# Optimization experiments

Hardware: AMD Instinct MI355X
Metric: run time of the kernel (lower is better)

Reference implementation:

```python
import jax, jax.numpy as jnp
import numpy as np

K = 10            # top-k patches
NUM_SAMPLES = 500 # perturbation samples
SIGMA = 0.05
PATCH = 128       # patch_size


def _perturbed_topk_core(x, noise):
    d = x.shape[-1]
    perturbed = x[:, None, :] + noise * SIGMA          # (b, n, d)
    _, idx = jax.lax.top_k(perturbed, K)               # (b, n, k)
    idx = jnp.sort(idx, axis=-1)
    onehot = jax.nn.one_hot(idx, d, dtype=x.dtype)     # (b, n, k, d)
    return onehot.mean(axis=1), onehot


@jax.custom_vjp
def perturbed_topk(x):
    noise = jax.random.normal(jax.random.key(1), (x.shape[0], NUM_SAMPLES, x.shape[1]), x.dtype)
    ind, _ = _perturbed_topk_core(x, noise)
    return ind


def _ptopk_fwd(x):
    noise = jax.random.normal(jax.random.key(1), (x.shape[0], NUM_SAMPLES, x.shape[1]), x.dtype)
    ind, onehot = _perturbed_topk_core(x, noise)
    return ind, (onehot, noise)


def _ptopk_bwd(res, g):
    onehot, noise = res
    # faithful to PerturbedTopKFunction.backward, fused to avoid the (b,k,d,e) tensor
    gx = jnp.einsum('bkd,bnkd,bne->be', g, onehot, noise) * (K / (NUM_SAMPLES * SIGMA))
    return (gx,)


perturbed_topk.defvjp(_ptopk_fwd, _ptopk_bwd)


def _forward(x_high, scores_2d):
    b, c, H, W = x_high.shape
    hs, ws = scores_2d.shape[1], scores_2d.shape[2]
    scores_1d = scores_2d.reshape(b, hs * ws)
    # entropy of softmax scores (torch.special.entr(p).sum(-1).mean(0))
    logp = jax.nn.log_softmax(scores_1d, axis=-1)
    p = jnp.exp(logp)
    entr = (-(p * logp).sum(-1)).mean()
    # min-max normalize
    smin = scores_1d.min(axis=-1, keepdims=True)
    smax = scores_1d.max(axis=-1, keepdims=True)
    norm = (scores_1d - smin) / (smax - smin + 1e-5)
    ind = perturbed_topk(norm).reshape(b, K, hs, ws)
    # padding identical to the torch code
    scale_h, scale_w = H // hs, W // ws
    padded_h = scale_h * hs + PATCH - 1
    padded_w = scale_w * ws + PATCH - 1
    top = (PATCH - scale_h) // 2
    left = (PATCH - scale_w) // 2
    bottom = padded_h - top - H
    right = padded_w - left - W
    x_pad = jnp.pad(x_high, ((0, 0), (0, 0), (top, bottom), (left, right)))
    # vectorized replacement of the nested i/j patch-accumulation loop
    row_idx = jnp.arange(hs)[:, None] * scale_h + jnp.arange(PATCH)[None, :]  # (hs, P)
    col_idx = jnp.arange(ws)[:, None] * scale_w + jnp.arange(PATCH)[None, :]  # (ws, P)
    # all candidate windows: (b, c, hs, ws, P, P)
    windows = x_pad[:, :, row_idx[:, None, :, None], col_idx[None, :, None, :]]
    patches = jnp.einsum('bcijhw,bkij->bkchw', windows, ind)  # (b, k, c, P, P)
    return patches, entr


def setup_inputs() -> dict:
    key = jax.random.key(0)
    k1, k2 = jax.random.split(key)
    x_high = jax.random.normal(k1, (8, 3, 1024, 1024), dtype=jnp.float32)
    scores_2d = jax.random.normal(k2, (8, 16, 16), dtype=jnp.float32)
    return {"x_high": x_high, "scores_2d": scores_2d}


def reference(x_high, scores_2d):
    return _forward(x_high, scores_2d)
```

## Files before the change

### kernel.cpp

```cpp
#include <hip/hip_runtime.h>
#include <stdint.h>

#define K_TOP 10
#define NSAMP 500
#define DIM 256
#define BATCH 8
#define WSTRIDE 12
#define PATCHES_ELEMS (8LL * 10 * 3 * 128 * 128)

__device__ __forceinline__ void threefry2x32_01(uint32_t x0, uint32_t x1,
                                                uint32_t& o0, uint32_t& o1) {
    const uint32_t ks0 = 0u;
    const uint32_t ks1 = 1u;
    const uint32_t ks2 = 0u ^ 1u ^ 0x1BD11BDAu;
    x0 += ks0; x1 += ks1;
#define TF_RND(r) { x0 += x1; x1 = (x1 << (r)) | (x1 >> (32 - (r))); x1 ^= x0; }
    TF_RND(13) TF_RND(15) TF_RND(26) TF_RND(6)
    x0 += ks1; x1 += ks2 + 1u;
    TF_RND(17) TF_RND(29) TF_RND(16) TF_RND(24)
    x0 += ks2; x1 += ks0 + 2u;
    TF_RND(13) TF_RND(15) TF_RND(26) TF_RND(6)
    x0 += ks0; x1 += ks1 + 3u;
    TF_RND(17) TF_RND(29) TF_RND(16) TF_RND(24)
    x0 += ks1; x1 += ks2 + 4u;
    TF_RND(13) TF_RND(15) TF_RND(26) TF_RND(6)
    x0 += ks2; x1 += ks0 + 5u;
#undef TF_RND
    o0 = x0; o1 = x1;
}

__device__ __forceinline__ float erfinv_xla(float x) {
    float w = -log1pf(-x * x);
    float p;
    if (w < 5.0f) {
        w = w - 2.5f;
        p = 2.81022636e-08f;
        p = fmaf(p, w, 3.43273939e-07f);
        p = fmaf(p, w, -3.5233877e-06f);
        p = fmaf(p, w, -4.39150654e-06f);
        p = fmaf(p, w, 0.00021858087f);
        p = fmaf(p, w, -0.00125372503f);
        p = fmaf(p, w, -0.00417768164f);
        p = fmaf(p, w, 0.246640727f);
        p = fmaf(p, w, 1.50140941f);
    } else {
        w = sqrtf(w) - 3.0f;
        p = -0.000200214257f;
        p = fmaf(p, w, 0.000100950558f);
        p = fmaf(p, w, 0.00134934322f);
        p = fmaf(p, w, -0.00367342844f);
        p = fmaf(p, w, 0.00573950773f);
        p = fmaf(p, w, -0.0076224613f);
        p = fmaf(p, w, 0.00943887047f);
        p = fmaf(p, w, 1.00167406f);
        p = fmaf(p, w, 2.83297682f);
    }
    return p * x;
}

__device__ __forceinline__ float jax_normal_at(uint32_t flat) {
    uint32_t o0, o1;
    threefry2x32_01(0u, flat, o0, o1);
    uint32_t bits = o0 ^ o1;
    float f = __uint_as_float((bits >> 9) | 0x3f800000u) - 1.0f;
    const float lo = -0.99999994f;
    float u = fmaxf(lo, fmaf(f, 2.0f, lo));
    return 1.4142135381698608f * erfinv_xla(u);
}

__global__ __launch_bounds__(256) void scores_kernel(
    const float* __restrict__ scores, float* __restrict__ norm,
    int* __restrict__ counts, float* __restrict__ entr_out) {
    __shared__ float s_ent[BATCH];
    const int tid = threadIdx.x;
    for (int i = tid; i < BATCH * K_TOP * DIM; i += 256) counts[i] = 0;
    const int wid = tid >> 6, lane = tid & 63;
#pragma unroll
    for (int bb = 0; bb < 2; ++bb) {
        const int b = wid * 2 + bb;
        const float s0 = scores[b * DIM + lane];
        const float s1 = scores[b * DIM + 64 + lane];
        const float s2 = scores[b * DIM + 128 + lane];
        const float s3 = scores[b * DIM + 192 + lane];
        float mx = fmaxf(fmaxf(s0, s1), fmaxf(s2, s3));
        float mn = fminf(fminf(s0, s1), fminf(s2, s3));
#pragma unroll
        for (int off = 1; off < 64; off <<= 1) {
            mx = fmaxf(mx, __shfl_xor(mx, off, 64));
            mn = fminf(mn, __shfl_xor(mn, off, 64));
        }
        const float e0 = expf(s0 - mx), e1 = expf(s1 - mx);
        const float e2 = expf(s2 - mx), e3 = expf(s3 - mx);
        float se = e0 + e1 + e2 + e3;
#pragma unroll
        for (int off = 1; off < 64; off <<= 1) se += __shfl_xor(se, off, 64);
        const float lse = logf(se);
        float pl = e0 * ((s0 - mx) - lse) + e1 * ((s1 - mx) - lse) +
                   e2 * ((s2 - mx) - lse) + e3 * ((s3 - mx) - lse);
#pragma unroll
        for (int off = 1; off < 64; off <<= 1) pl += __shfl_xor(pl, off, 64);
        if (lane == 0) s_ent[b] = -(pl / se);
        const float den = mx - mn + 1e-5f;
        norm[b * DIM + lane]        = (s0 - mn) / den;
        norm[b * DIM + 64 + lane]   = (s1 - mn) / den;
        norm[b * DIM + 128 + lane]  = (s2 - mn) / den;
        norm[b * DIM + 192 + lane]  = (s3 - mn) / den;
    }
    __syncthreads();
    if (tid == 0) {
        float acc = 0.f;
#pragma unroll
        for (int b = 0; b < BATCH; ++b) acc += s_ent[b];
        entr_out[0] = acc * 0.125f;
    }
}

__global__ __launch_bounds__(256) void topk_kernel(
    const float* __restrict__ norm, int* __restrict__ counts) {
    const int wid = threadIdx.x >> 6;
    const int lane = threadIdx.x & 63;
    const int r = blockIdx.x * 4 + wid;
    const int b = r / NSAMP;

    const uint32_t base = (uint32_t)r * 256u;
    float v0 = norm[b * DIM + lane]       + jax_normal_at(base + (uint32_t)lane)         * 0.05f;
    float v1 = norm[b * DIM + 64 + lane]  + jax_normal_at(base + 64u + (uint32_t)lane)   * 0.05f;
    float v2 = norm[b * DIM + 128 + lane] + jax_normal_at(base + 128u + (uint32_t)lane)  * 0.05f;
    float v3 = norm[b * DIM + 192 + lane] + jax_normal_at(base + 192u + (uint32_t)lane)  * 0.05f;

    int chosen[K_TOP];
#pragma unroll
    for (int it = 0; it < K_TOP; ++it) {
        float bv = v0; int bd = lane;
        { int d = 64 + lane;  if (v1 > bv || (v1 == bv && d < bd)) { bv = v1; bd = d; } }
        { int d = 128 + lane; if (v2 > bv || (v2 == bv && d < bd)) { bv = v2; bd = d; } }
        { int d = 192 + lane; if (v3 > bv || (v3 == bv && d < bd)) { bv = v3; bd = d; } }
#pragma unroll
        for (int off = 1; off < 64; off <<= 1) {
            float ov = __shfl_xor(bv, off, 64);
            int   od = __shfl_xor(bd, off, 64);
            if (ov > bv || (ov == bv && od < bd)) { bv = ov; bd = od; }
        }
        chosen[it] = bd;
        if ((bd & 63) == lane) {
            int q = bd >> 6;
            if (q == 0) v0 = -__builtin_inff();
            else if (q == 1) v1 = -__builtin_inff();
            else if (q == 2) v2 = -__builtin_inff();
            else v3 = -__builtin_inff();
        }
    }
#pragma unroll
    for (int a = 0; a < K_TOP - 1; ++a)
#pragma unroll
        for (int t = 0; t < K_TOP - 1 - a; ++t) {
            int x0 = chosen[t], x1 = chosen[t + 1];
            chosen[t] = min(x0, x1);
            chosen[t + 1] = max(x0, x1);
        }
    if (lane == 0) {
        const int cb = b * K_TOP * DIM;
#pragma unroll
        for (int k = 0; k < K_TOP; ++k)
            atomicAdd(&counts[cb + (k << 8) + chosen[k]], 1);
    }
}

__global__ __launch_bounds__(64) void compact_union_kernel(
    const int* __restrict__ counts, int* __restrict__ u_ij,
    float* __restrict__ u_wt, int* __restrict__ u_n) {
    const int b = blockIdx.x;
    const int lane = threadIdx.x;
    int any0 = 0, any1 = 0, any2 = 0, any3 = 0;
    const int d0 = lane * 4;
#pragma unroll
    for (int k = 0; k < K_TOP; ++k) {
        const int* cb = counts + (b * K_TOP + k) * DIM;
        any0 |= cb[d0 + 0];
        any1 |= cb[d0 + 1];
        any2 |= cb[d0 + 2];
        any3 |= cb[d0 + 3];
    }
    int n = (any0 > 0) + (any1 > 0) + (any2 > 0) + (any3 > 0);
    int incl = n;
#pragma unroll
    for (int off = 1; off < 64; off <<= 1) {
        int t = __shfl_up(incl, off, 64);
        if (lane >= off) incl += t;
    }
    int pos = b * DIM + (incl - n);
#define EMIT(ANY, DD)                                                        \
    if (ANY > 0) {                                                           \
        u_ij[pos] = (DD);                                                    \
        _Pragma("unroll")                                                    \
        for (int k = 0; k < K_TOP; ++k)                                      \
            u_wt[pos * K_TOP + k] =                                          \
                (float)counts[(b * K_TOP + k) * DIM + (DD)] / 500.0f;        \
        pos++;                                                               \
    }
    EMIT(any0, d0 + 0)
    EMIT(any1, d0 + 1)
    EMIT(any2, d0 + 2)
    EMIT(any3, d0 + 3)
#undef EMIT
    if (lane == 63) u_n[b] = incl;
}

__device__ __forceinline__ void fma10(float4 acc[K_TOP], const float4 v,
                                      const float* __restrict__ w12) {
    const float4 wA = *(const float4*)(w12);
    const float4 wB = *(const float4*)(w12 + 4);
    const float2 wC = *(const float2*)(w12 + 8);
    const float wk[K_TOP] = {wA.x, wA.y, wA.z, wA.w,
                             wB.x, wB.y, wB.z, wB.w, wC.x, wC.y};
#pragma unroll
    for (int k = 0; k < K_TOP; ++k) {
        acc[k].x = fmaf(wk[k], v.x, acc[k].x);
        acc[k].y = fmaf(wk[k], v.y, acc[k].y);
        acc[k].z = fmaf(wk[k], v.z, acc[k].z);
        acc[k].w = fmaf(wk[k], v.w, acc[k].w);
    }
}

__global__ __launch_bounds__(256) void gather_kernel(
    const float* __restrict__ x, const int* __restrict__ u_ij,
    const float* __restrict__ u_wt, const int* __restrict__ u_n,
    float* __restrict__ out) {
    __shared__ float4 ldsbuf[2][K_TOP][64];
    int*   s_ij = (int*)&ldsbuf[0][0][0];
    float* s_wt = (float*)(s_ij + DIM);

    const int blk = blockIdx.x;
    const int rc = blk & 63;
    const int bc = blk >> 6;
    const int b = bc / 3;
    const int c = bc % 3;
    const int nnz = u_n[b];
    const int tid = threadIdx.x;
    const int wid = tid >> 6, lane = tid & 63;
    const int h = (rc << 1) + (lane >> 5);
    const int w0 = (lane & 31) << 2;
    const float* img = x + (size_t)bc * (1024 * 1024);

    for (int i = tid; i < nnz; i += 256) s_ij[i] = u_ij[b * DIM + i];
    for (int i = tid; i < nnz * K_TOP; i += 256) {
        const int t = i / K_TOP, k = i - t * K_TOP;
        s_wt[t * WSTRIDE + k] = u_wt[b * DIM * K_TOP + i];
    }
    __syncthreads();

    float4 acc[K_TOP];
#pragma unroll
    for (int k = 0; k < K_TOP; ++k) acc[k] = make_float4(0.f, 0.f, 0.f, 0.f);

    for (int t0 = wid * 2; t0 < nnz; t0 += 8) {
        const int t1 = t0 + 1;
        const int ij0 = s_ij[t0];
        const int y0  = (ij0 >> 4) * 64 + h - 32;
        const int xc0 = (ij0 & 15) * 64 + w0 - 32;
        float4 v0 = make_float4(0.f, 0.f, 0.f, 0.f);
        if ((unsigned)y0 < 1024u && (unsigned)xc0 < 1024u)
            v0 = *(const float4*)(img + ((size_t)y0 << 10) + xc0);

        if (t1 < nnz) {
            const int ij1 = s_ij[t1];
            const int y1  = (ij1 >> 4) * 64 + h - 32;
            const int xc1 = (ij1 & 15) * 64 + w0 - 32;
            float4 v1 = make_float4(0.f, 0.f, 0.f, 0.f);
            if ((unsigned)y1 < 1024u && (unsigned)xc1 < 1024u)
                v1 = *(const float4*)(img + ((size_t)y1 << 10) + xc1);
            fma10(acc, v0, &s_wt[t0 * WSTRIDE]);
            fma10(acc, v1, &s_wt[t1 * WSTRIDE]);
        } else {
            fma10(acc, v0, &s_wt[t0 * WSTRIDE]);
        }
    }

    __syncthreads();
    if (wid >= 2) {
#pragma unroll
        for (int k = 0; k < K_TOP; ++k) ldsbuf[wid - 2][k][lane] = acc[k];
    }
    __syncthreads();
    if (wid < 2) {
#pragma unroll
        for (int k = 0; k < K_TOP; ++k) {
            const float4 t = ldsbuf[wid][k][lane];
            acc[k].x += t.x; acc[k].y += t.y; acc[k].z += t.z; acc[k].w += t.w;
        }
    }
    __syncthreads();
    if (wid == 1) {
#pragma unroll
        for (int k = 0; k < K_TOP; ++k) ldsbuf[0][k][lane] = acc[k];
    }
    __syncthreads();
    if (wid == 0) {
#pragma unroll
        for (int k = 0; k < K_TOP; ++k) {
            const float4 t = ldsbuf[0][k][lane];
            acc[k].x += t.x; acc[k].y += t.y; acc[k].z += t.z; acc[k].w += t.w;
            const size_t oidx =
                (((size_t)((b * K_TOP + k) * 3 + c)) << 14) + (h << 7) + w0;
            *(float4*)(out + oidx) = acc[k];
        }
    }
}

extern "C" void kernel_launch(void* const* d_in, const int* in_sizes, int n_in,
                              void* d_out, int out_size, void* d_ws,
                              size_t ws_size, hipStream_t stream) {
    const float* x_high = (const float*)d_in[0];
    const float* scores = (const float*)d_in[1];
    float* out = (float*)d_out;

    float* norm  = (float*)d_ws;
    int*   counts = (int*)(norm + BATCH * DIM);
    int*   u_ij  = counts + BATCH * K_TOP * DIM;
    float* u_wt  = (float*)(u_ij + BATCH * DIM);
    int*   u_n   = (int*)(u_wt + BATCH * DIM * K_TOP);

    scores_kernel<<<1, 256, 0, stream>>>(scores, norm, counts,
                                         out + PATCHES_ELEMS);
    topk_kernel<<<1000, 256, 0, stream>>>(norm, counts);
    compact_union_kernel<<<BATCH, 64, 0, stream>>>(counts, u_ij, u_wt, u_n);
    gather_kernel<<<BATCH * 3 * 64, 256, 0, stream>>>(x_high, u_ij, u_wt, u_n,
                                                      out);
}
```

Before: 171.9 us.

## Fuse score normalization and union compaction into topk and gather kernels

Removes the scores and compaction kernels, cutting the pipeline from four launches to two. The topk kernel now computes the min-max normalization itself and writes raw per-sample indices without global atomics. Each gather block rebuilds the per-batch histogram in LDS and compacts the union with a block-wide scan, and one extra block computes the entropy. This removes launch overhead and serial tiny kernels, but every gather block redoes the histogram work over 5000 indices, which is redundant.

```diff
diff --git a/kernel.cpp b/kernel.cpp
--- a/kernel.cpp
+++ b/kernel.cpp
@@ -68,65 +68,31 @@
     return 1.4142135381698608f * erfinv_xla(u);
 }
 
-__global__ __launch_bounds__(256) void scores_kernel(
-    const float* __restrict__ scores, float* __restrict__ norm,
-    int* __restrict__ counts, float* __restrict__ entr_out) {
-    __shared__ float s_ent[BATCH];
-    const int tid = threadIdx.x;
-    for (int i = tid; i < BATCH * K_TOP * DIM; i += 256) counts[i] = 0;
-    const int wid = tid >> 6, lane = tid & 63;
-#pragma unroll
-    for (int bb = 0; bb < 2; ++bb) {
-        const int b = wid * 2 + bb;
-        const float s0 = scores[b * DIM + lane];
-        const float s1 = scores[b * DIM + 64 + lane];
-        const float s2 = scores[b * DIM + 128 + lane];
-        const float s3 = scores[b * DIM + 192 + lane];
-        float mx = fmaxf(fmaxf(s0, s1), fmaxf(s2, s3));
-        float mn = fminf(fminf(s0, s1), fminf(s2, s3));
-#pragma unroll
-        for (int off = 1; off < 64; off <<= 1) {
-            mx = fmaxf(mx, __shfl_xor(mx, off, 64));
-            mn = fminf(mn, __shfl_xor(mn, off, 64));
-        }
-        const float e0 = expf(s0 - mx), e1 = expf(s1 - mx);
-        const float e2 = expf(s2 - mx), e3 = expf(s3 - mx);
-        float se = e0 + e1 + e2 + e3;
-#pragma unroll
-        for (int off = 1; off < 64; off <<= 1) se += __shfl_xor(se, off, 64);
-        const float lse = logf(se);
-        float pl = e0 * ((s0 - mx) - lse) + e1 * ((s1 - mx) - lse) +
-                   e2 * ((s2 - mx) - lse) + e3 * ((s3 - mx) - lse);
-#pragma unroll
-        for (int off = 1; off < 64; off <<= 1) pl += __shfl_xor(pl, off, 64);
-        if (lane == 0) s_ent[b] = -(pl / se);
-        const float den = mx - mn + 1e-5f;
-        norm[b * DIM + lane]        = (s0 - mn) / den;
-        norm[b * DIM + 64 + lane]   = (s1 - mn) / den;
-        norm[b * DIM + 128 + lane]  = (s2 - mn) / den;
-        norm[b * DIM + 192 + lane]  = (s3 - mn) / den;
-    }
-    __syncthreads();
-    if (tid == 0) {
-        float acc = 0.f;
-#pragma unroll
-        for (int b = 0; b < BATCH; ++b) acc += s_ent[b];
-        entr_out[0] = acc * 0.125f;
-    }
-}
-
 __global__ __launch_bounds__(256) void topk_kernel(
-    const float* __restrict__ norm, int* __restrict__ counts) {
+    const float* __restrict__ scores, int* __restrict__ topk_out) {
     const int wid = threadIdx.x >> 6;
     const int lane = threadIdx.x & 63;
     const int r = blockIdx.x * 4 + wid;
     const int b = r / NSAMP;
 
+    const float s0 = scores[b * DIM + lane];
+    const float s1 = scores[b * DIM + 64 + lane];
+    const float s2 = scores[b * DIM + 128 + lane];
+    const float s3 = scores[b * DIM + 192 + lane];
+    float mx = fmaxf(fmaxf(s0, s1), fmaxf(s2, s3));
+    float mn = fminf(fminf(s0, s1), fminf(s2, s3));
+#pragma unroll
+    for (int off = 1; off < 64; off <<= 1) {
+        mx = fmaxf(mx, __shfl_xor(mx, off, 64));
+        mn = fminf(mn, __shfl_xor(mn, off, 64));
+    }
+    const float den = mx - mn + 1e-5f;
+
     const uint32_t base = (uint32_t)r * 256u;
-    float v0 = norm[b * DIM + lane]       + jax_normal_at(base + (uint32_t)lane)         * 0.05f;
-    float v1 = norm[b * DIM + 64 + lane]  + jax_normal_at(base + 64u + (uint32_t)lane)   * 0.05f;
-    float v2 = norm[b * DIM + 128 + lane] + jax_normal_at(base + 128u + (uint32_t)lane)  * 0.05f;
-    float v3 = norm[b * DIM + 192 + lane] + jax_normal_at(base + 192u + (uint32_t)lane)  * 0.05f;
+    float v0 = (s0 - mn) / den + jax_normal_at(base + (uint32_t)lane)        * 0.05f;
+    float v1 = (s1 - mn) / den + jax_normal_at(base + 64u + (uint32_t)lane)  * 0.05f;
+    float v2 = (s2 - mn) / den + jax_normal_at(base + 128u + (uint32_t)lane) * 0.05f;
+    float v3 = (s3 - mn) / den + jax_normal_at(base + 192u + (uint32_t)lane) * 0.05f;
 
     int chosen[K_TOP];
 #pragma unroll
@@ -159,51 +125,10 @@
             chosen[t + 1] = max(x0, x1);
         }
     if (lane == 0) {
-        const int cb = b * K_TOP * DIM;
-#pragma unroll
-        for (int k = 0; k < K_TOP; ++k)
-            atomicAdd(&counts[cb + (k << 8) + chosen[k]], 1);
-    }
-}
-
-__global__ __launch_bounds__(64) void compact_union_kernel(
-    const int* __restrict__ counts, int* __restrict__ u_ij,
-    float* __restrict__ u_wt, int* __restrict__ u_n) {
-    const int b = blockIdx.x;
-    const int lane = threadIdx.x;
-    int any0 = 0, any1 = 0, any2 = 0, any3 = 0;
-    const int d0 = lane * 4;
-#pragma unroll
-    for (int k = 0; k < K_TOP; ++k) {
-        const int* cb = counts + (b * K_TOP + k) * DIM;
-        any0 |= cb[d0 + 0];
-        any1 |= cb[d0 + 1];
-        any2 |= cb[d0 + 2];
-        any3 |= cb[d0 + 3];
-    }
-    int n = (any0 > 0) + (any1 > 0) + (any2 > 0) + (any3 > 0);
-    int incl = n;
-#pragma unroll
-    for (int off = 1; off < 64; off <<= 1) {
-        int t = __shfl_up(incl, off, 64);
-        if (lane >= off) incl += t;
-    }
-    int pos = b * DIM + (incl - n);
-#define EMIT(ANY, DD)                                                        \
-    if (ANY > 0) {                                                           \
-        u_ij[pos] = (DD);                                                    \
-        _Pragma("unroll")                                                    \
-        for (int k = 0; k < K_TOP; ++k)                                      \
-            u_wt[pos * K_TOP + k] =                                          \
-                (float)counts[(b * K_TOP + k) * DIM + (DD)] / 500.0f;        \
-        pos++;                                                               \
-    }
-    EMIT(any0, d0 + 0)
-    EMIT(any1, d0 + 1)
-    EMIT(any2, d0 + 2)
-    EMIT(any3, d0 + 3)
-#undef EMIT
-    if (lane == 63) u_n[b] = incl;
+        int* row = topk_out + r * K_TOP;
+#pragma unroll
+        for (int k = 0; k < K_TOP; ++k) row[k] = chosen[k];
+    }
 }
 
 __device__ __forceinline__ void fma10(float4 acc[K_TOP], const float4 v,
@@ -223,29 +148,92 @@
 }
 
 __global__ __launch_bounds__(256) void gather_kernel(
-    const float* __restrict__ x, const int* __restrict__ u_ij,
-    const float* __restrict__ u_wt, const int* __restrict__ u_n,
-    float* __restrict__ out) {
+    const float* __restrict__ x, const float* __restrict__ scores,
+    const int* __restrict__ topk_out, float* __restrict__ out) {
     __shared__ float4 ldsbuf[2][K_TOP][64];
+    __shared__ int wsum[4];
+    __shared__ float s_ent[BATCH];
+    int*   hist = (int*)&ldsbuf[0][0][0];
     int*   s_ij = (int*)&ldsbuf[0][0][0];
     float* s_wt = (float*)(s_ij + DIM);
+
+    const int tid = threadIdx.x;
+    const int wid = tid >> 6, lane = tid & 63;
+
+    if (blockIdx.x == BATCH * 3 * 64) {
+#pragma unroll
+        for (int bb = 0; bb < 2; ++bb) {
+            const int b = wid * 2 + bb;
+            const float s0 = scores[b * DIM + lane];
+            const float s1 = scores[b * DIM + 64 + lane];
+            const float s2 = scores[b * DIM + 128 + lane];
+            const float s3 = scores[b * DIM + 192 + lane];
+            float mx = fmaxf(fmaxf(s0, s1), fmaxf(s2, s3));
+#pragma unroll
+            for (int off = 1; off < 64; off <<= 1)
+                mx = fmaxf(mx, __shfl_xor(mx, off, 64));
+            const float e0 = expf(s0 - mx), e1 = expf(s1 - mx);
+            const float e2 = expf(s2 - mx), e3 = expf(s3 - mx);
+            float se = e0 + e1 + e2 + e3;
+#pragma unroll
+            for (int off = 1; off < 64; off <<= 1) se += __shfl_xor(se, off, 64);
+            const float lse = logf(se);
+            float pl = e0 * ((s0 - mx) - lse) + e1 * ((s1 - mx) - lse) +
+                       e2 * ((s2 - mx) - lse) + e3 * ((s3 - mx) - lse);
+#pragma unroll
+            for (int off = 1; off < 64; off <<= 1) pl += __shfl_xor(pl, off, 64);
+            if (lane == 0) s_ent[b] = -(pl / se);
+        }
+        __syncthreads();
+        if (tid == 0) {
+            float acc = 0.f;
+#pragma unroll
+            for (int b = 0; b < BATCH; ++b) acc += s_ent[b];
+            out[PATCHES_ELEMS] = acc * 0.125f;
+        }
+        return;
+    }
 
     const int blk = blockIdx.x;
     const int rc = blk & 63;
     const int bc = blk >> 6;
     const int b = bc / 3;
     const int c = bc % 3;
-    const int nnz = u_n[b];
-    const int tid = threadIdx.x;
-    const int wid = tid >> 6, lane = tid & 63;
     const int h = (rc << 1) + (lane >> 5);
     const int w0 = (lane & 31) << 2;
     const float* img = x + (size_t)bc * (1024 * 1024);
 
-    for (int i = tid; i < nnz; i += 256) s_ij[i] = u_ij[b * DIM + i];
-    for (int i = tid; i < nnz * K_TOP; i += 256) {
-        const int t = i / K_TOP, k = i - t * K_TOP;
-        s_wt[t * WSTRIDE + k] = u_wt[b * DIM * K_TOP + i];
+    for (int i = tid; i < K_TOP * DIM; i += 256) hist[i] = 0;
+    __syncthreads();
+    const int* tk = topk_out + b * NSAMP * K_TOP;
+    for (int i = tid; i < NSAMP * K_TOP; i += 256) {
+        const int k = i % K_TOP;
+        atomicAdd(&hist[k * DIM + tk[i]], 1);
+    }
+    __syncthreads();
+
+    int cnt[K_TOP]; int any = 0;
+#pragma unroll
+    for (int k = 0; k < K_TOP; ++k) { cnt[k] = hist[k * DIM + tid]; any |= cnt[k]; }
+    const int flag = any ? 1 : 0;
+    int incl = flag;
+#pragma unroll
+    for (int off = 1; off < 64; off <<= 1) {
+        int t = __shfl_up(incl, off, 64);
+        if (lane >= off) incl += t;
+    }
+    if (lane == 63) wsum[wid] = incl;
+    __syncthreads();
+    int woff = 0;
+#pragma unroll
+    for (int w = 0; w < 4; ++w) if (w < wid) woff += wsum[w];
+    const int nnz = wsum[0] + wsum[1] + wsum[2] + wsum[3];
+    if (flag) {
+        const int pos = woff + incl - flag;
+        s_ij[pos] = tid;
+#pragma unroll
+        for (int k = 0; k < K_TOP; ++k)
+            s_wt[pos * WSTRIDE + k] = (float)cnt[k] / 500.0f;
     }
     __syncthreads();
 
@@ -314,16 +302,9 @@
     const float* scores = (const float*)d_in[1];
     float* out = (float*)d_out;
 
-    float* norm  = (float*)d_ws;
-    int*   counts = (int*)(norm + BATCH * DIM);
-    int*   u_ij  = counts + BATCH * K_TOP * DIM;
-    float* u_wt  = (float*)(u_ij + BATCH * DIM);
-    int*   u_n   = (int*)(u_wt + BATCH * DIM * K_TOP);
-
-    scores_kernel<<<1, 256, 0, stream>>>(scores, norm, counts,
-                                         out + PATCHES_ELEMS);
-    topk_kernel<<<1000, 256, 0, stream>>>(norm, counts);
-    compact_union_kernel<<<BATCH, 64, 0, stream>>>(counts, u_ij, u_wt, u_n);
-    gather_kernel<<<BATCH * 3 * 64, 256, 0, stream>>>(x_high, u_ij, u_wt, u_n,
-                                                      out);
-}
+    int* topk_out = (int*)d_ws;
+
+    topk_kernel<<<1000, 256, 0, stream>>>(scores, topk_out);
+    gather_kernel<<<BATCH * 3 * 64 + 1, 256, 0, stream>>>(x_high, scores,
+                                                          topk_out, out);
+}
```

Measured after the change: 165.5 us. 3.7% less time.
